# Kernel optimization log

Measured on AMD Instinct MI355X. Metric: run time of the kernel, lower is better.

Reference implementation:

```python
import jax, jax.numpy as jnp
import numpy as np

EPS = 1e-5  # BatchNorm eps (torch default)


def setup_inputs() -> dict:
    key = jax.random.key(0)
    ks = jax.random.split(key, 12)
    B, T, F = 2048, 128, 84

    def rn(k, sh, scale=0.05):
        return jax.random.normal(k, sh, jnp.float32) * scale

    return {
        "x": jax.random.normal(ks[0], (B, T, F), jnp.float32),
        # Conv1d(84 -> 64, k=3, pad=1)
        "conv1d_w": rn(ks[1], (64, F, 3)),
        "conv1d_b": rn(ks[2], (64,)),
        # BatchNorm1d(64), eval mode (running stats)
        "bn_gamma": jnp.ones((64,), jnp.float32),
        "bn_beta": jnp.zeros((64,), jnp.float32),
        "bn_mean": jnp.zeros((64,), jnp.float32),
        "bn_var": jnp.ones((64,), jnp.float32),
        # Linear(64*16 -> 64*4*4)
        "lin_w": rn(ks[3], (1024, 1024)),
        "lin_b": rn(ks[4], (1024,)),
        # ConvLSTM cell: Conv2d(192 -> 512, k=3, pad=1, groups=4)
        "cell_w": rn(ks[5], (512, 48, 3, 3)),
        "cell_b": rn(ks[6], (512,)),
        # Classifier
        "cls1_w": rn(ks[7], (128, 2048)),
        "cls1_b": rn(ks[8], (128,)),
        "cls2_w": rn(ks[9], (2, 128)),
        "cls2_b": rn(ks[10], (2,)),
    }


def reference(x, conv1d_w, conv1d_b, bn_gamma, bn_beta, bn_mean, bn_var,
              lin_w, lin_b, cell_w, cell_b, cls1_w, cls1_b, cls2_w, cls2_b):
    B, T, F = x.shape
    H = 128  # hidden channels

    # Per-timestep encoder is state-free -> vectorize over (B, T).
    # Conv1d k=3 pad=1 on a length-1 sequence: only the center tap hits data.
    enc = jnp.einsum('btf,cf->btc', x, conv1d_w[:, :, 1]) + conv1d_b  # [B,T,64]
    enc = (enc - bn_mean) * (bn_gamma / jnp.sqrt(bn_var + EPS)) + bn_beta
    enc = jax.nn.relu(enc)
    # flatten of [64,16] is channel-major -> repeat along last axis.
    flat = jnp.repeat(enc, 16, axis=-1)                               # [B,T,1024]
    to2d = jnp.einsum('btk,ok->bto', flat, lin_w) + lin_b             # [B,T,1024]
    xt = to2d.reshape(B, T, 64, 4, 4).transpose(1, 0, 2, 3, 4)        # [T,B,64,4,4]

    def step(carry, x_t):
        h, c = carry
        comb = jnp.concatenate([x_t, h], axis=1)                      # [B,192,4,4]
        conv = jax.lax.conv_general_dilated(
            comb, cell_w, window_strides=(1, 1), padding='SAME',
            dimension_numbers=('NCHW', 'OIHW', 'NCHW'),
            feature_group_count=4)
        conv = conv + cell_b[None, :, None, None]                     # [B,512,4,4]
        cc_i, cc_f, cc_o, cc_g = jnp.split(conv, 4, axis=1)
        c_next = jax.nn.sigmoid(cc_f) * c + jax.nn.sigmoid(cc_i) * jnp.tanh(cc_g)
        h_next = jax.nn.sigmoid(cc_o) * jnp.tanh(c_next)
        return (h_next, c_next), None

    h0 = jnp.zeros((B, H, 4, 4), x.dtype)
    (h_last, _), _ = jax.lax.scan(step, (h0, h0), xt)

    feat = h_last.reshape(B, H * 16)                                  # [B,2048]
    hid = jax.nn.relu(feat @ cls1_w.T + cls1_b)
    return hid @ cls2_w.T + cls2_b                                    # [B,2]
```

## Files before the change

### kernel.cpp

```cpp
#include <hip/hip_runtime.h>
#include <math.h>

#define BN_EPS 1e-5f

typedef _Float16 f16x8 __attribute__((ext_vector_type(8)));
typedef _Float16 f16x4 __attribute__((ext_vector_type(4)));
typedef _Float16 f16x2 __attribute__((ext_vector_type(2)));
typedef unsigned short u16x8 __attribute__((ext_vector_type(8)));
typedef float f32x4 __attribute__((ext_vector_type(4)));
typedef float f32x16 __attribute__((ext_vector_type(16)));


__global__ void prep_enc_w(const float* __restrict__ conv1d_w,
                           const float* __restrict__ conv1d_b,
                           const float* __restrict__ gamma,
                           const float* __restrict__ beta,
                           const float* __restrict__ mean,
                           const float* __restrict__ var,
                           float* __restrict__ We, float* __restrict__ be) {
  int tid = blockIdx.x * blockDim.x + threadIdx.x;
  if (tid < 5376) {
    int c = tid / 84, f = tid % 84;
    float s = gamma[c] * rsqrtf(var[c] + BN_EPS);
    We[c * 84 + f] = s * conv1d_w[c * 252 + f * 3 + 1];
    if (f == 0) be[c] = s * conv1d_b[c] + (beta[c] - mean[c] * s);
  }
}

__global__ void prep_wef(const float* __restrict__ We, _Float16* __restrict__ WeF) {
  int tid = blockIdx.x * blockDim.x + threadIdx.x;
  if (tid >= 6144) return;
  int j = tid & 7, lane = (tid >> 3) & 63, kch = (tid >> 9) % 3, ct = tid / 1536;
  int c = ct * 16 + (lane & 15);
  int k = kch * 32 + (lane >> 4) * 8 + j;
  WeF[tid] = (k < 84) ? (_Float16)We[c * 84 + k] : (_Float16)0.f;
}

__global__ void prep_w2(const float* __restrict__ lin_w, float* __restrict__ W2) {
  int tid = blockIdx.x * blockDim.x + threadIdx.x;
  int o2 = tid >> 6, c = tid & 63;
  float s = 0.f;
#pragma unroll
  for (int j = 0; j < 16; ++j) s += lin_w[o2 * 1024 + c * 16 + j];
  W2[o2 * 64 + c] = s;
}

__global__ void prep_A(const float* __restrict__ cell_w,
                       const float* __restrict__ cell_b,
                       const float* __restrict__ lin_b,
                       const float* __restrict__ W2,
                       float* __restrict__ A, float* __restrict__ Abias) {
  int tid = blockIdx.x * blockDim.x + threadIdx.x;
  int go = tid >> 10;
  int c = (tid >> 4) & 63;
  int p = tid & 15;
  int y = p >> 2, x = p & 3;
  int kn = (go >= 128) ? 16 : 48;
  int xb = (go >= 128) ? 48 : 0;
  float a = 0.f;
  for (int k = 0; k < kn; ++k)
    for (int dy = 0; dy < 3; ++dy) {
      int yy = y + dy - 1;
      if (yy < 0 || yy > 3) continue;
      for (int dx = 0; dx < 3; ++dx) {
        int xx = x + dx - 1;
        if (xx < 0 || xx > 3) continue;
        a += cell_w[((go * 48 + k) * 3 + dy) * 3 + dx] *
             W2[((xb + k) * 16 + yy * 4 + xx) * 64 + c];
      }
    }
  A[(go * 64 + c) * 16 + p] = a;
  if (c == 0) {
    float bs = cell_b[go];
    for (int k = 0; k < kn; ++k)
      for (int dy = 0; dy < 3; ++dy) {
        int yy = y + dy - 1;
        if (yy < 0 || yy > 3) continue;
        for (int dx = 0; dx < 3; ++dx) {
          int xx = x + dx - 1;
          if (xx < 0 || xx > 3) continue;
          bs += cell_w[((go * 48 + k) * 3 + dy) * 3 + dx] *
                lin_b[(xb + k) * 16 + yy * 4 + xx];
        }
      }
    Abias[go * 16 + p] = bs;
  }
}

__global__ void pack_a16(const float* __restrict__ A, _Float16* __restrict__ Apk) {
  int tid = blockIdx.x * blockDim.x + threadIdx.x;
  int j = tid & 7, lane = (tid >> 3) & 63, kch = (tid >> 9) & 1, go = tid >> 10;
  int p = lane & 15;
  int c = kch * 32 + (lane >> 4) * 8 + j;
  Apk[tid] = (_Float16)A[(go * 64 + c) * 16 + p];
}

__global__ void pack_wcv(const float* __restrict__ cell_w, _Float16* __restrict__ Wcv) {
  int tid = blockIdx.x * blockDim.x + threadIdx.x;
  int j = tid & 7, lane = (tid >> 3) & 63, m = (tid >> 9) & 3, tmk = tid >> 11;
  int co = m * 32 + (lane & 31);
  int khi = (lane >> 5) * 8 + j;
  float v;
  if (tmk < 18) {
    int kch = tmk / 9, tap = tmk % 9;
    v = cell_w[((size_t)(128 + co) * 48 + 16 + kch * 16 + khi) * 9 + tap];
  } else if (tmk < 45) {
    int r = tmk - 18; int kch = r / 9, tap = r % 9;
    v = cell_w[((size_t)(256 + co) * 48 + kch * 16 + khi) * 9 + tap];
  } else {
    int r = tmk - 45; int kch = r / 9, tap = r % 9;
    v = cell_w[((size_t)(384 + co) * 48 + kch * 16 + khi) * 9 + tap];
  }
  Wcv[tid] = (_Float16)v;
}

__device__ __forceinline__ float sigm(float v) {
  return __fdividef(1.f, 1.f + __expf(-v));
}
__device__ __forceinline__ float tanh_fast(float v) {
  return 1.f - __fdividef(2.f, __expf(2.f * v) + 1.f);
}

__global__ __launch_bounds__(256, 3) void xgate_kernel(
    const float* __restrict__ x, const _Float16* __restrict__ WeF,
    const float* __restrict__ be, const _Float16* __restrict__ Apk,
    const float* __restrict__ Abias, unsigned short* __restrict__ sixf, int tc) {
  __shared__ __align__(16) _Float16 x16[128 * 104];
  __shared__ __align__(16) _Float16 enc_s[128 * 72];
  __shared__ __align__(16) unsigned char Tt[4 * 2304];
  int tid = threadIdx.x, lane = tid & 63, w = tid >> 6;
  int gq = blockIdx.x >> 7, cq = blockIdx.x & 127;
  int n = lane & 15, kgrp = lane >> 4;

  {
    int r = tid >> 1, half = tid & 1;
    int b = cq * 16 + (r >> 3), t = tc * 8 + (r & 7);
    const float* rowp = x + ((size_t)b * 128 + t) * 84;
#pragma unroll
    for (int j = 0; j < 11; ++j) {
      int q = half + 2 * j;
      if (q < 21) {
        float4 v = *(const float4*)(rowp + q * 4);
        f16x4 h;
        h[0] = (_Float16)v.x; h[1] = (_Float16)v.y;
        h[2] = (_Float16)v.z; h[3] = (_Float16)v.w;
        *(f16x4*)(&x16[r * 104 + q * 4]) = h;
      }
    }
    for (int i = tid; i < 4096; i += 256) {
      int rr = i >> 5, k = i & 31;
      if (k < 20) x16[rr * 104 + 84 + k] = (_Float16)0.f;
    }
  }
  __syncthreads();

  for (int ct4 = 0; ct4 < 8; ++ct4) {
    f32x4 acc = *(const f32x4*)(be + w * 16 + kgrp * 4);
#pragma unroll
    for (int kch = 0; kch < 3; ++kch)
      acc = __builtin_amdgcn_mfma_f32_16x16x32_f16(
          *(const f16x8*)(WeF + ((w * 3 + kch) * 64 + lane) * 8),
          *(const f16x8*)(&x16[(ct4 * 16 + n) * 104 + kch * 32 + kgrp * 8]),
          acc, 0, 0, 0);
#pragma unroll
    for (int r = 0; r < 4; ++r)
      enc_s[(ct4 * 16 + n) * 72 + w * 16 + kgrp * 4 + r] =
          (_Float16)fmaxf(acc[r], 0.f);
  }
  __syncthreads();

  int slotB = gq >> 1;
  int chbase = (gq & 1) * 64 + w * 16;
  unsigned char* Tw = Tt + w * 2304;
  int fn = lane >> 2;
  for (int ct4 = 0; ct4 < 8; ++ct4) {
    int ccl = ct4 * 16 + n;
    int fb = cq * 16 + ct4 * 2 + (fn >> 3), ftr = fn & 7;
    size_t grow =
        (((size_t)fb * 8 + ftr) * 2 + slotB) * 2048 + (size_t)chbase * 16;
    for (int gb = 0; gb < 4; ++gb) {
#pragma unroll
      for (int gi = 0; gi < 4; ++gi) {
        int gol = gb * 4 + gi;
        int go = gq * 64 + w * 16 + gol;
        f32x4 acc = *(const f32x4*)(Abias + go * 16 + kgrp * 4);
        acc = __builtin_amdgcn_mfma_f32_16x16x32_f16(
            *(const f16x8*)(Apk + (size_t)go * 1024 + lane * 8),
            *(const f16x8*)(&enc_s[ccl * 72 + kgrp * 8]), acc, 0, 0, 0);
        acc = __builtin_amdgcn_mfma_f32_16x16x32_f16(
            *(const f16x8*)(Apk + (size_t)go * 1024 + 512 + lane * 8),
            *(const f16x8*)(&enc_s[ccl * 72 + 32 + kgrp * 8]), acc, 0, 0, 0);
        unsigned char* tdst = Tw + n * 144 + gi * 32 + kgrp * 8;
        if (gq < 2) {
#pragma unroll
          for (int rp = 0; rp < 2; ++rp) {
            unsigned lo = (unsigned)(sigm(acc[rp * 2]) * 65535.f + 0.5f);
            unsigned hi = (unsigned)(sigm(acc[rp * 2 + 1]) * 65535.f + 0.5f);
            *(unsigned*)(tdst + rp * 4) = lo | (hi << 16);
          }
        } else {
#pragma unroll
          for (int rp = 0; rp < 2; ++rp) {
            f16x2 pv = {(_Float16)acc[rp * 2], (_Float16)acc[rp * 2 + 1]};
            *(f16x2*)(tdst + rp * 4) = pv;
          }
        }
      }
      asm volatile("s_waitcnt lgkmcnt(0)" ::: "memory");
      __builtin_amdgcn_sched_barrier(0);
#pragma unroll
      for (int j = 0; j < 2; ++j) {
        int chunk = (lane & 3) + 4 * j;
        f16x8 v = *(const f16x8*)(Tw + fn * 144 + chunk * 16);
        *(f16x8*)(sixf + grow + (size_t)gb * 64 + (size_t)chunk * 8) = v;
      }
      asm volatile("s_waitcnt lgkmcnt(0)" ::: "memory");
      __builtin_amdgcn_sched_barrier(0);
    }
  }
}

#define HPB 4624
#define HPQ 272
#define ZQ 4352
#define COFF 36992
#define GOFF 102528
#define GSZ 18432
#define LDSZ 157824

__device__ __forceinline__ void vupdate(
    unsigned char* lds, const unsigned short* __restrict__ sixf_b,
    _Float16* __restrict__ h16_b, int ch, int blbit, int h8,
    float cbo, float cbg, int q) {
  int tP = q >> 2, hfP = (q >> 1) & 1, ntP = q & 1;
  int b = hfP * 4 + ntP * 2 + blbit;
  bool lastT = (tP == 7);
  const unsigned short* sp =
      sixf_b + ((size_t)b * 8 + tP) * 4096 + ch * 16 + h8 * 8;
  u16x8 s = *(const u16x8*)sp;
  f16x8 xv = *(const f16x8*)(sp + 2048);
  unsigned gbyte = (unsigned)(ch * 144 + ntP * 64 + blbit * 32 + h8 * 16);
  f16x8 gfv = *(const f16x8*)(lds + GOFF + 0 * GSZ + gbyte);
  f16x8 gov = *(const f16x8*)(lds + GOFF + 1 * GSZ + gbyte);
  f16x8 ggv = *(const f16x8*)(lds + GOFF + 2 * GSZ + gbyte);
  float* cp = (float*)(lds + COFF) +
              (((hfP * 2 + ntP) * 256 + blbit * 128 + ch) * 16 + h8 * 8);
#pragma unroll
  for (int j = 0; j < 8; ++j) {
    int p = h8 * 8 + j;
    float si = (float)s[j] * (1.f / 65535.f);
    float cv = sigm((float)xv[j] + (float)gfv[j]) * cp[j] +
               si * tanh_fast(cbg + (float)ggv[j]);
    cp[j] = cv;
    float hn = sigm(cbo + (float)gov[j]) * tanh_fast(cv);
    *(_Float16*)(lds + b * HPB + p * HPQ + ch * 2) = (_Float16)hn;
    if (lastT) h16_b[((size_t)b * 16 + p) * 128 + ch] = (_Float16)hn;
  }
}

template <int GATE>
__device__ __forceinline__ void role_loop(
    unsigned char* lds, const _Float16* __restrict__ Wg,
    const unsigned short* __restrict__ sixf_b,
    _Float16* __restrict__ h16_b,
    int m, int lane, int tid, const unsigned* tapbase, unsigned gwbase,
    int ch_u, int blbit_u, int h8_u, float cbo, float cbg) {
  constexpr int NKCH = (GATE == 0) ? 2 : 3;
  constexpr unsigned CIOFF = (GATE == 0) ? 0u : (GATE == 1 ? 64u : 160u);
  f16x8 wr[NKCH * 9];
#pragma unroll
  for (int fi = 0; fi < NKCH * 9; ++fi)
    wr[fi] = *(const f16x8*)(Wg + (size_t)(fi * 4 + m) * 512 + (lane << 3));

  for (int q = 0; q < 32; ++q) {
    if (q > 0) {
      int ntP = (q - 1) & 1;
      bool own = (GATE == 0) || (GATE == 1 && ntP == 0) || (GATE == 2 && ntP == 1);
      if (own)
        vupdate(lds, sixf_b, h16_b, ch_u, blbit_u, h8_u, cbo, cbg, q - 1);
    }
    int hf = (q >> 1) & 1, nt = q & 1;
    unsigned bofs = (unsigned)(hf * 4 + nt * 2) * HPB;
    f32x16 acc = {};
#pragma unroll
    for (int kch = 0; kch < NKCH; ++kch)
#pragma unroll
      for (int tap = 0; tap < 9; ++tap)
        acc = __builtin_amdgcn_mfma_f32_32x32x16_f16(
            wr[kch * 9 + tap],
            *(const f16x8*)(lds + tapbase[tap] + bofs + CIOFF +
                            (unsigned)kch * 32),
            acc, 0, 0, 0);
#pragma unroll
    for (int r = 0; r < 16; ++r) {
      unsigned co_l = (unsigned)((r & 3) + 8 * (r >> 2));
      *(_Float16*)(lds + gwbase + (unsigned)GATE * GSZ + co_l * 144u +
                   (unsigned)nt * 64u) = (_Float16)acc[r];
    }
    __syncthreads();
  }
  if (GATE == 0 || GATE == 2)
    vupdate(lds, sixf_b, h16_b, ch_u, blbit_u, h8_u, cbo, cbg, 31);
  __syncthreads();
}

__global__ __launch_bounds__(768, 3) void recur8_kernel(
    const unsigned short* __restrict__ sixf, const _Float16* __restrict__ Wcv,
    const float* __restrict__ cell_b, _Float16* __restrict__ h16,
    float* __restrict__ cstate) {
  __shared__ __align__(16) unsigned char lds[LDSZ];
  int tid = threadIdx.x, lane = tid & 63, w = tid >> 6;
  int gate = w >> 2, m = w & 3;

  _Float16* h16_b = h16 + (size_t)blockIdx.x * 16384;
  for (int i = tid; i < 16384; i += 768) {
    int bl8 = i >> 11, q = (i >> 7) & 15, chh = i & 127;
    *(_Float16*)(lds + bl8 * HPB + q * HPQ + chh * 2) = h16_b[i];
  }
  for (int i = tid; i < 1024; i += 768) {
    int bl8 = i >> 7, chh = i & 127;
    *(_Float16*)(lds + bl8 * HPB + ZQ + chh * 2) = (_Float16)0.f;
  }
  float* cl = (float*)(lds + COFF);
  float* cst_b = cstate + (size_t)blockIdx.x * 16384;
  for (int i = tid; i < 16384; i += 768) cl[i] = cst_b[i];

  int task = (gate == 2) ? (tid - 256) : tid;
  int ch_u = task >> 2, blbit_u = (task >> 1) & 1, h8_u = task & 1;
  float cbo = cell_b[256 + ch_u], cbg = cell_b[384 + ch_u];

  int col = lane & 31, khalf = lane >> 5, b_lo = col >> 4, p_c = col & 15;
  int yc = p_c >> 2, xc = p_c & 3;
  unsigned tapbase[9];
#pragma unroll
  for (int dy = 0; dy < 3; ++dy)
#pragma unroll
    for (int dx = 0; dx < 3; ++dx) {
      int qy = yc + dy - 1, qx = xc + dx - 1;
      bool valid = (qy >= 0 && qy < 4 && qx >= 0 && qx < 4);
      tapbase[dy * 3 + dx] =
          (valid ? (unsigned)((qy * 4 + qx) * HPQ) : (unsigned)ZQ) +
          (unsigned)(b_lo * HPB + khalf * 16);
    }
  unsigned gwbase = (unsigned)GOFF + (unsigned)((m * 32 + khalf * 4) * 144) +
                    (unsigned)(b_lo * 32 + p_c * 2);
  __syncthreads();

  const unsigned short* sixf_b = sixf + (size_t)blockIdx.x * 262144;
  if (gate == 0)
    role_loop<0>(lds, Wcv, sixf_b, h16_b, m, lane, tid, tapbase, gwbase,
                 ch_u, blbit_u, h8_u, cbo, cbg);
  else if (gate == 1)
    role_loop<1>(lds, Wcv + 36864, sixf_b, h16_b, m, lane, tid, tapbase, gwbase,
                 ch_u, blbit_u, h8_u, cbo, cbg);
  else
    role_loop<2>(lds, Wcv + 92160, sixf_b, h16_b, m, lane, tid, tapbase, gwbase,
                 ch_u, blbit_u, h8_u, cbo, cbg);

  for (int i = tid; i < 16384; i += 768) cst_b[i] = cl[i];
}

__global__ __launch_bounds__(128) void cls_kernel(
    const _Float16* __restrict__ h16, const float* __restrict__ w1,
    const float* __restrict__ b1, const float* __restrict__ w2,
    const float* __restrict__ b2, float* __restrict__ out) {
  __shared__ __align__(16) float feat[8 * 2064];
  __shared__ float hid[8 * 128];
  int b0 = blockIdx.x * 8;
  for (int i = threadIdx.x; i < 16384; i += 128) {
    int bl = i >> 11, r = i & 2047, p = r >> 7, chh = r & 127;
    feat[bl * 2064 + chh * 16 + p] = (float)h16[(size_t)b0 * 2048 + i];
  }
  __syncthreads();
  int ch = threadIdx.x;
  float acc[8];
#pragma unroll
  for (int b = 0; b < 8; ++b) acc[b] = b1[ch];
  const float4* wr = (const float4*)(w1 + (size_t)ch * 2048);
  for (int k4 = 0; k4 < 512; ++k4) {
    float4 wv = wr[k4];
#pragma unroll
    for (int b = 0; b < 8; ++b) {
      float4 f = *(const float4*)(&feat[b * 2064 + k4 * 4]);
      acc[b] += wv.x * f.x + wv.y * f.y + wv.z * f.z + wv.w * f.w;
    }
  }
#pragma unroll
  for (int b = 0; b < 8; ++b) hid[b * 128 + ch] = fmaxf(acc[b], 0.f);
  __syncthreads();
  if (threadIdx.x < 16) {
    int b = threadIdx.x >> 1, o = threadIdx.x & 1;
    float s = b2[o];
    for (int k = 0; k < 128; ++k) s += hid[b * 128 + k] * w2[o * 128 + k];
    out[(size_t)(b0 + b) * 2 + o] = s;
  }
}

extern "C" void kernel_launch(void* const* d_in, const int* in_sizes, int n_in,
                              void* d_out, int out_size, void* d_ws, size_t ws_size,
                              hipStream_t stream) {
  const float* x        = (const float*)d_in[0];
  const float* conv1d_w = (const float*)d_in[1];
  const float* conv1d_b = (const float*)d_in[2];
  const float* bn_gamma = (const float*)d_in[3];
  const float* bn_beta  = (const float*)d_in[4];
  const float* bn_mean  = (const float*)d_in[5];
  const float* bn_var   = (const float*)d_in[6];
  const float* lin_w    = (const float*)d_in[7];
  const float* lin_b    = (const float*)d_in[8];
  const float* cell_w   = (const float*)d_in[9];
  const float* cell_b   = (const float*)d_in[10];
  const float* cls1_w   = (const float*)d_in[11];
  const float* cls1_b   = (const float*)d_in[12];
  const float* cls2_w   = (const float*)d_in[13];
  const float* cls2_b   = (const float*)d_in[14];

  float* ws = (float*)d_ws;
  float* We    = ws + 0;
  float* be    = ws + 8192;
  float* W2    = ws + 12288;
  float* A     = ws + 81920;
  float* Abias = ws + 344064;
  _Float16* WeF = (_Float16*)(ws + 348160);
  _Float16* Apk = (_Float16*)(ws + 352256);
  _Float16* Wcv = (_Float16*)(ws + 483328);
  _Float16* h16 = (_Float16*)(ws + 557056);
  float* cstate = ws + 2654208;
  unsigned short* sixf = (unsigned short*)(ws + 6848512);
  float* out = (float*)d_out;

  prep_enc_w<<<21, 256, 0, stream>>>(conv1d_w, conv1d_b, bn_gamma, bn_beta,
                                     bn_mean, bn_var, We, be);
  prep_wef<<<24, 256, 0, stream>>>(We, WeF);
  prep_w2<<<256, 256, 0, stream>>>(lin_w, W2);
  prep_A<<<1024, 256, 0, stream>>>(cell_w, cell_b, lin_b, W2, A, Abias);
  pack_a16<<<1024, 256, 0, stream>>>(A, Apk);
  pack_wcv<<<576, 256, 0, stream>>>(cell_w, Wcv);
  hipMemsetAsync(h16, 0, 8388608, stream);
  hipMemsetAsync(cstate, 0, 16777216, stream);
  for (int tc = 0; tc < 16; ++tc) {
    xgate_kernel<<<512, 256, 0, stream>>>(x, WeF, be, Apk, Abias, sixf, tc);
    recur8_kernel<<<256, 768, 0, stream>>>(sixf, Wcv, cell_b, h16, cstate);
  }
  cls_kernel<<<256, 128, 0, stream>>>(h16, cls1_w, cls1_b, cls2_w, cls2_b, out);
}
```

Before: 3.593 ms.

## Halve batch per recurrence block to launch 512 blocks with smaller LDS

The recurrent ConvLSTM kernel now processes 4 batch elements per block instead of 8, halving LDS usage and doubling the grid to 512 blocks, with launch bounds raised to allow more resident blocks. The per-step schedule changes from a software-pipelined 32-iteration loop that overlapped the previous tile's cell update with the next MFMA tile to a plain loop with two barriers per half, where gate ownership splits the cell update. This aims to fill more CUs on the 256-CU device and shorten the serial chain per block. In exchange it gives up the MFMA/elementwise overlap and adds barriers.

Measured after the change: 7.768 ms. +116.2%, slower.

```diff
diff --git a/kernel.cpp b/kernel.cpp
--- a/kernel.cpp
+++ b/kernel.cpp
@@ -223,35 +223,34 @@
 #define HPB 4624
 #define HPQ 272
 #define ZQ 4352
-#define COFF 36992
-#define GOFF 102528
-#define GSZ 18432
-#define LDSZ 157824
-
-__device__ __forceinline__ void vupdate(
+#define COFF 18496
+#define GOFF 51264
+#define GSZ 9216
+#define LDSZ 78912
+
+__device__ __forceinline__ void cell_update(
     unsigned char* lds, const unsigned short* __restrict__ sixf_b,
-    _Float16* __restrict__ h16_b, int ch, int blbit, int h8,
-    float cbo, float cbg, int q) {
-  int tP = q >> 2, hfP = (q >> 1) & 1, ntP = q & 1;
-  int b = hfP * 4 + ntP * 2 + blbit;
-  bool lastT = (tP == 7);
+    _Float16* __restrict__ h16_b, int ch, int bl, int h8, int hf, int t,
+    float cbo, float cbg, bool lastT) {
+  int b = hf * 2 + bl;
+  int cell = ch * 4 + b;
   const unsigned short* sp =
-      sixf_b + ((size_t)b * 8 + tP) * 4096 + ch * 16 + h8 * 8;
+      sixf_b + ((size_t)b * 8 + t) * 4096 + ch * 16 + h8 * 8;
   u16x8 s = *(const u16x8*)sp;
   f16x8 xv = *(const f16x8*)(sp + 2048);
-  unsigned gbyte = (unsigned)(ch * 144 + ntP * 64 + blbit * 32 + h8 * 16);
+  unsigned gbyte = (unsigned)(ch * 72 + bl * 32 + h8 * 16);
   f16x8 gfv = *(const f16x8*)(lds + GOFF + 0 * GSZ + gbyte);
   f16x8 gov = *(const f16x8*)(lds + GOFF + 1 * GSZ + gbyte);
   f16x8 ggv = *(const f16x8*)(lds + GOFF + 2 * GSZ + gbyte);
-  float* cp = (float*)(lds + COFF) +
-              (((hfP * 2 + ntP) * 256 + blbit * 128 + ch) * 16 + h8 * 8);
+  float* cl = (float*)(lds + COFF);
 #pragma unroll
   for (int j = 0; j < 8; ++j) {
     int p = h8 * 8 + j;
     float si = (float)s[j] * (1.f / 65535.f);
-    float cv = sigm((float)xv[j] + (float)gfv[j]) * cp[j] +
+    float* cp = cl + p * 512 + cell;
+    float cv = sigm((float)xv[j] + (float)gfv[j]) * cp[0] +
                si * tanh_fast(cbg + (float)ggv[j]);
-    cp[j] = cv;
+    cp[0] = cv;
     float hn = sigm(cbo + (float)gov[j]) * tanh_fast(cv);
     *(_Float16*)(lds + b * HPB + p * HPQ + ch * 2) = (_Float16)hn;
     if (lastT) h16_b[((size_t)b * 16 + p) * 128 + ch] = (_Float16)hn;
@@ -264,7 +263,7 @@
     const unsigned short* __restrict__ sixf_b,
     _Float16* __restrict__ h16_b,
     int m, int lane, int tid, const unsigned* tapbase, unsigned gwbase,
-    int ch_u, int blbit_u, int h8_u, float cbo, float cbg) {
+    int ch_u, int bl_u, int h8_u, float cbo, float cbg) {
   constexpr int NKCH = (GATE == 0) ? 2 : 3;
   constexpr unsigned CIOFF = (GATE == 0) ? 0u : (GATE == 1 ? 64u : 160u);
   f16x8 wr[NKCH * 9];
@@ -272,39 +271,44 @@
   for (int fi = 0; fi < NKCH * 9; ++fi)
     wr[fi] = *(const f16x8*)(Wg + (size_t)(fi * 4 + m) * 512 + (lane << 3));
 
-  for (int q = 0; q < 32; ++q) {
-    if (q > 0) {
-      int ntP = (q - 1) & 1;
-      bool own = (GATE == 0) || (GATE == 1 && ntP == 0) || (GATE == 2 && ntP == 1);
-      if (own)
-        vupdate(lds, sixf_b, h16_b, ch_u, blbit_u, h8_u, cbo, cbg, q - 1);
-    }
-    int hf = (q >> 1) & 1, nt = q & 1;
-    unsigned bofs = (unsigned)(hf * 4 + nt * 2) * HPB;
-    f32x16 acc = {};
-#pragma unroll
-    for (int kch = 0; kch < NKCH; ++kch)
-#pragma unroll
-      for (int tap = 0; tap < 9; ++tap)
-        acc = __builtin_amdgcn_mfma_f32_32x32x16_f16(
-            wr[kch * 9 + tap],
-            *(const f16x8*)(lds + tapbase[tap] + bofs + CIOFF +
-                            (unsigned)kch * 32),
-            acc, 0, 0, 0);
-#pragma unroll
-    for (int r = 0; r < 16; ++r) {
-      unsigned co_l = (unsigned)((r & 3) + 8 * (r >> 2));
-      *(_Float16*)(lds + gwbase + (unsigned)GATE * GSZ + co_l * 144u +
-                   (unsigned)nt * 64u) = (_Float16)acc[r];
-    }
-    __syncthreads();
-  }
-  if (GATE == 0 || GATE == 2)
-    vupdate(lds, sixf_b, h16_b, ch_u, blbit_u, h8_u, cbo, cbg, 31);
-  __syncthreads();
-}
-
-__global__ __launch_bounds__(768, 3) void recur8_kernel(
+  constexpr bool own0 = (GATE != 2), own1 = (GATE != 1);
+
+  for (int t = 0; t < 8; ++t) {
+#pragma unroll
+    for (int hf = 0; hf < 2; ++hf) {
+      unsigned bofs = (unsigned)(hf * 2) * HPB;
+      f32x16 acc = {};
+#pragma unroll
+      for (int kch = 0; kch < NKCH; ++kch)
+#pragma unroll
+        for (int tap = 0; tap < 9; ++tap)
+          acc = __builtin_amdgcn_mfma_f32_32x32x16_f16(
+              wr[kch * 9 + tap],
+              *(const f16x8*)(lds + tapbase[tap] + bofs + CIOFF +
+                              (unsigned)kch * 32),
+              acc, 0, 0, 0);
+#pragma unroll
+      for (int r = 0; r < 16; ++r) {
+        unsigned co_l = (unsigned)((r & 3) + 8 * (r >> 2));
+        *(_Float16*)(lds + gwbase + (unsigned)GATE * GSZ + co_l * 72u) =
+            (_Float16)acc[r];
+      }
+      __syncthreads();
+      if (hf == 0) {
+        if (own0)
+          cell_update(lds, sixf_b, h16_b, ch_u, bl_u, h8_u, 0, t, cbo, cbg,
+                      t == 7);
+      } else {
+        if (own1)
+          cell_update(lds, sixf_b, h16_b, ch_u, bl_u, h8_u, 1, t, cbo, cbg,
+                      t == 7);
+      }
+      __syncthreads();
+    }
+  }
+}
+
+__global__ __launch_bounds__(768, 6) void recur8_kernel(
     const unsigned short* __restrict__ sixf, const _Float16* __restrict__ Wcv,
     const float* __restrict__ cell_b, _Float16* __restrict__ h16,
     float* __restrict__ cstate) {
@@ -312,21 +316,21 @@
   int tid = threadIdx.x, lane = tid & 63, w = tid >> 6;
   int gate = w >> 2, m = w & 3;
 
-  _Float16* h16_b = h16 + (size_t)blockIdx.x * 16384;
-  for (int i = tid; i < 16384; i += 768) {
-    int bl8 = i >> 11, q = (i >> 7) & 15, chh = i & 127;
-    *(_Float16*)(lds + bl8 * HPB + q * HPQ + chh * 2) = h16_b[i];
-  }
-  for (int i = tid; i < 1024; i += 768) {
-    int bl8 = i >> 7, chh = i & 127;
-    *(_Float16*)(lds + bl8 * HPB + ZQ + chh * 2) = (_Float16)0.f;
+  _Float16* h16_b = h16 + (size_t)blockIdx.x * 8192;
+  for (int i = tid; i < 8192; i += 768) {
+    int bl4 = i >> 11, q = (i >> 7) & 15, chh = i & 127;
+    *(_Float16*)(lds + bl4 * HPB + q * HPQ + chh * 2) = h16_b[i];
+  }
+  for (int i = tid; i < 512; i += 768) {
+    int bl4 = i >> 7, chh = i & 127;
+    *(_Float16*)(lds + bl4 * HPB + ZQ + chh * 2) = (_Float16)0.f;
   }
   float* cl = (float*)(lds + COFF);
-  float* cst_b = cstate + (size_t)blockIdx.x * 16384;
-  for (int i = tid; i < 16384; i += 768) cl[i] = cst_b[i];
-
-  int task = (gate == 2) ? (tid - 256) : tid;
-  int ch_u = task >> 2, blbit_u = (task >> 1) & 1, h8_u = task & 1;
+  float* cst_b = cstate + (size_t)blockIdx.x * 8192;
+  for (int i = tid; i < 8192; i += 768) cl[i] = cst_b[i];
+
+  int idx = (gate == 2) ? (tid - 256) : tid;
+  int ch_u = idx >> 2, bl_u = (idx >> 1) & 1, h8_u = idx & 1;
   float cbo = cell_b[256 + ch_u], cbg = cell_b[384 + ch_u];
 
   int col = lane & 31, khalf = lane >> 5, b_lo = col >> 4, p_c = col & 15;
@@ -342,22 +346,22 @@
           (valid ? (unsigned)((qy * 4 + qx) * HPQ) : (unsigned)ZQ) +
           (unsigned)(b_lo * HPB + khalf * 16);
     }
-  unsigned gwbase = (unsigned)GOFF + (unsigned)((m * 32 + khalf * 4) * 144) +
+  unsigned gwbase = (unsigned)GOFF + (unsigned)((m * 32 + khalf * 4) * 72) +
                     (unsigned)(b_lo * 32 + p_c * 2);
   __syncthreads();
 
-  const unsigned short* sixf_b = sixf + (size_t)blockIdx.x * 262144;
+  const unsigned short* sixf_b = sixf + (size_t)blockIdx.x * 131072;
   if (gate == 0)
     role_loop<0>(lds, Wcv, sixf_b, h16_b, m, lane, tid, tapbase, gwbase,
-                 ch_u, blbit_u, h8_u, cbo, cbg);
+                 ch_u, bl_u, h8_u, cbo, cbg);
   else if (gate == 1)
-    role_loop<1>(lds, Wcv + 36864, sixf_b, h16_b, m, lane, tid, tapbase, gwbase,
-                 ch_u, blbit_u, h8_u, cbo, cbg);
+    role_loop<1>(lds, Wcv + 36864, sixf_b, h16_b, m, lane, tid, tapbase,
+                 gwbase, ch_u, bl_u, h8_u, cbo, cbg);
   else
-    role_loop<2>(lds, Wcv + 92160, sixf_b, h16_b, m, lane, tid, tapbase, gwbase,
-                 ch_u, blbit_u, h8_u, cbo, cbg);
-
-  for (int i = tid; i < 16384; i += 768) cst_b[i] = cl[i];
+    role_loop<2>(lds, Wcv + 92160, sixf_b, h16_b, m, lane, tid, tapbase,
+                 gwbase, ch_u, bl_u, h8_u, cbo, cbg);
+
+  for (int i = tid; i < 8192; i += 768) cst_b[i] = cl[i];
 }
 
 __global__ __launch_bounds__(128) void cls_kernel(
@@ -440,7 +444,7 @@
   hipMemsetAsync(cstate, 0, 16777216, stream);
   for (int tc = 0; tc < 16; ++tc) {
     xgate_kernel<<<512, 256, 0, stream>>>(x, WeF, be, Apk, Abias, sixf, tc);
-    recur8_kernel<<<256, 768, 0, stream>>>(sixf, Wcv, cell_b, h16, cstate);
+    recur8_kernel<<<512, 768, 0, stream>>>(sixf, Wcv, cell_b, h16, cstate);
   }
   cls_kernel<<<256, 128, 0, stream>>>(h16, cls1_w, cls1_b, cls2_w, cls2_b, out);
 }
```
